# Performance work log

Measured on AMD Instinct MI355X. Metric: run time of the kernel, lower is better.

## Reference

```python
import jax, jax.numpy as jnp
import numpy as np
import math

H = 128          # node_dim == hidden_dim
TED = 128        # time_emb_dim
T = 64
BN = 4096


def _mlp(x, w1, b1, w2, b2):
    # 2-layer MLP with SiLU, matching MLP(n_layer=2, act_fn=SiLU)
    return jax.nn.silu(x @ w1 + b1) @ w2 + b2


def _timestep_embedding(t, dim):
    # get_timestep_embedding for possibly-negative relative indices
    half = dim // 2
    freqs = jnp.exp(jnp.arange(half, dtype=jnp.float32) * (-math.log(10000.0) / (half - 1)))
    arg = t.astype(jnp.float32)[:, None] * freqs[None, :]
    return jnp.concatenate([jnp.sin(arg), jnp.cos(arg)], axis=-1)


def setup_inputs() -> dict:
    key = jax.random.key(0)
    ks = jax.random.split(key, 20)
    s = 1.0 / math.sqrt(H)
    d = {
        "x": jax.random.normal(ks[0], (BN, 3, T), jnp.float32),
        "h": jax.random.normal(ks[1], (BN, H, T), jnp.float32),
        "q_w1": jax.random.normal(ks[2], (H, H), jnp.float32) * s,
        "q_b1": jnp.zeros((H,), jnp.float32),
        "q_w2": jax.random.normal(ks[3], (H, H), jnp.float32) * s,
        "q_b2": jnp.zeros((H,), jnp.float32),
        "k_w1": jax.random.normal(ks[4], (H, H), jnp.float32) * s,
        "k_b1": jnp.zeros((H,), jnp.float32),
        "k_w2": jax.random.normal(ks[5], (H, H), jnp.float32) * s,
        "k_b2": jnp.zeros((H,), jnp.float32),
        "v_w1": jax.random.normal(ks[6], (H, H), jnp.float32) * s,
        "v_b1": jnp.zeros((H,), jnp.float32),
        "v_w2": jax.random.normal(ks[7], (H, H), jnp.float32) * s,
        "v_b2": jnp.zeros((H,), jnp.float32),
        "xm_w1": jax.random.normal(ks[8], (H, H), jnp.float32) * s,
        "xm_b1": jnp.zeros((H,), jnp.float32),
        "xm_w2": jax.random.normal(ks[9], (H, 1), jnp.float32) * s,
        "xm_b2": jnp.zeros((1,), jnp.float32),
        "t_w": jax.random.normal(ks[10], (TED, H), jnp.float32) * (1.0 / math.sqrt(TED)),
        "t_b": jnp.zeros((H,), jnp.float32),
    }
    return d


def reference(x, h, q_w1, q_b1, q_w2, q_b2, k_w1, k_b1, k_w2, k_b2,
              v_w1, v_b1, v_w2, v_b2, xm_w1, xm_b1, xm_w2, xm_b2, t_w, t_b):
    Tn = x.shape[-1]
    # relative time embedding E[t, s, :] of shape [T, T, H]
    ti = jnp.arange(Tn)
    rel = (ti[:, None] - ti[None, :]).reshape(-1)
    E = (_timestep_embedding(rel, TED) @ t_w + t_b).reshape(Tn, Tn, -1)

    # merge_time_dim: [N, H, T] -> [N*T, H]  (token order: node-major, time-minor)
    tok = h.transpose(0, 2, 1)                      # [N, T, H]
    q = _mlp(tok, q_w1, q_b1, q_w2, q_b2)           # [N, T, H]
    k = _mlp(tok, k_w1, k_b1, k_w2, k_b2)           # [N, T, H]
    v = _mlp(tok, v_w1, v_b1, v_w2, v_b2)           # [N, T, H]
    vx = _mlp(v, xm_w1, xm_b1, xm_w2, xm_b2)[..., 0]  # [N, T]

    # scores: q . (k_s + E_ts)  -- decomposed, avoids materializing k_ts [N,H,T,T]
    scores = jnp.einsum('nth,nsh->nts', q, k) + jnp.einsum('nth,tsh->nts', q, E)
    alpha = jax.nn.softmax(scores, axis=-1)          # [N, T, S]

    # h update: sum_s alpha * (v_s + E_ts)
    dh = jnp.einsum('nts,nsh->nth', alpha, v) + jnp.einsum('nts,tsh->nth', alpha, E)
    h_out = h + dh.transpose(0, 2, 1)                # [N, H, T]

    # x update: x_t += sum_s alpha[t,s] * vx[s] * (x_t - x_s)
    w = alpha * vx[:, None, :]                       # [N, T, S]
    x_out = x + x * jnp.sum(w, axis=-1)[:, None, :] - jnp.einsum('nts,nds->ndt', w, x)
    return (x_out, h_out)
```

## Files before the change

kernel.cpp:

```cpp
#include <hip/hip_runtime.h>
#include <hip/hip_bf16.h>
#include <math.h>

#define NN 4096

typedef __attribute__((ext_vector_type(8))) short s8v;
typedef __attribute__((ext_vector_type(4))) float f4v;
typedef __attribute__((ext_vector_type(4))) unsigned int u32x4;
typedef __attribute__((ext_vector_type(2))) unsigned int u32x2;
typedef unsigned short u16;

static __device__ __forceinline__ f4v MFMA16(s8v a, s8v b, f4v c) {
  return __builtin_amdgcn_mfma_f32_16x16x32_bf16(a, b, c, 0, 0, 0);
}
static __device__ __forceinline__ u16 f2bf(float f) {
  union { float f; unsigned int u; } v; v.f = f;
  unsigned int r = v.u + 0x7fffu + ((v.u >> 16) & 1u);
  return (u16)(r >> 16);
}
static __device__ __forceinline__ float bf2f(u16 u) {
  union { unsigned int u; float f; } v; v.u = ((unsigned int)u) << 16;
  return v.f;
}
static __device__ __forceinline__ unsigned int cvt2u(float lo, float hi) {
  __hip_bfloat162 h = __float22bfloat162_rn(make_float2(lo, hi));
  union { __hip_bfloat162 b; unsigned int u; } c; c.b = h; return c.u;
}

#define SW(row, byte)  ((row) * 256 + ((byte) ^ (((row) & 7) << 4)))
#define SWH(row, byte) ((row) * 128 + ((byte) ^ (((row) & 7) << 4)))

__global__ void prep_kernel(const float* __restrict__ qw1, const float* __restrict__ qw2,
                            const float* __restrict__ kw1, const float* __restrict__ kw2,
                            const float* __restrict__ vw1, const float* __restrict__ vw2,
                            const float* __restrict__ xmw1,
                            const float* __restrict__ t_w, const float* __restrict__ t_b,
                            u16* __restrict__ wsb) {
  int b = blockIdx.x;
  if (b < 7) {
    const float* W;
    switch (b) {
      case 0: W = qw1; break; case 1: W = qw2; break;
      case 2: W = kw1; break; case 3: W = kw2; break;
      case 4: W = vw1; break; case 5: W = vw2; break;
      default: W = xmw1; break;
    }
    u16* o = wsb + b * 16384;
    for (int i = 0; i < 128; ++i) {
      int idx = i * 128 + threadIdx.x;
      int h = idx >> 7, c = idx & 127;
      o[c * 128 + h] = f2bf(W[idx]);
    }
  } else {
    int r = b - 7;
    int o = threadIdx.x;
    __shared__ float sc[128];
    float rel = (float)(r - 63);
    if (o < 64) {
      float f = expf((float)o * (-logf(10000.0f) / 63.0f));
      float a = rel * f;
      sc[o] = sinf(a);
      sc[o + 64] = cosf(a);
    }
    __syncthreads();
    float acc = t_b[o];
    for (int i = 0; i < 128; ++i) acc = fmaf(sc[i], t_w[i * 128 + o], acc);
    u16 bb = f2bf(acc);
    wsb[7 * 16384 + r * 128 + o] = bb;
    wsb[8 * 16384 + o * 128 + r] = bb;
  }
}

template <bool SILU, bool HASB, bool VT>
__device__ __forceinline__ void gemm128(const u16* __restrict__ Ag,
                                        const unsigned char* Bl,
                                        unsigned char* Ol,
                                        unsigned char* vTout,
                                        const float* __restrict__ bias,
                                        int w, int l) {
  const int lr = l & 15, lk = l >> 4;
  const int m0 = w * 16;
  float bj[4];
#pragma unroll
  for (int j = 0; j < 4; ++j) bj[j] = HASB ? bias[m0 + lk * 4 + j] : 0.f;
  f4v acc[4];
#pragma unroll
  for (int ni = 0; ni < 4; ++ni)
#pragma unroll
    for (int j = 0; j < 4; ++j) acc[ni][j] = bj[j];
#pragma unroll
  for (int kt = 0; kt < 4; ++kt) {
    s8v a = *(const s8v*)&Ag[(m0 + lr) * 128 + kt * 32 + lk * 8];
#pragma unroll
    for (int ni = 0; ni < 4; ++ni) {
      s8v b = *(const s8v*)(Bl + SW(ni * 16 + lr, kt * 64 + lk * 16));
      acc[ni] = MFMA16(a, b, acc[ni]);
    }
  }
#pragma unroll
  for (int ni = 0; ni < 4; ++ni) {
    int t = ni * 16 + lr;
    float v0 = acc[ni][0], v1 = acc[ni][1], v2 = acc[ni][2], v3 = acc[ni][3];
    if (SILU) {
      v0 *= __builtin_amdgcn_rcpf(1.0f + __expf(-v0));
      v1 *= __builtin_amdgcn_rcpf(1.0f + __expf(-v1));
      v2 *= __builtin_amdgcn_rcpf(1.0f + __expf(-v2));
      v3 *= __builtin_amdgcn_rcpf(1.0f + __expf(-v3));
    }
    unsigned int c0 = cvt2u(v0, v1), c1 = cvt2u(v2, v3);
    u32x2 st; st[0] = c0; st[1] = c1;
    *(u32x2*)(Ol + SW(t, m0 * 2 + lk * 8)) = st;
    if (VT) {
      *(u16*)(vTout + SWH(m0 + lk * 4 + 0, t * 2)) = (u16)(c0 & 0xffffu);
      *(u16*)(vTout + SWH(m0 + lk * 4 + 1, t * 2)) = (u16)(c0 >> 16);
      *(u16*)(vTout + SWH(m0 + lk * 4 + 2, t * 2)) = (u16)(c1 & 0xffffu);
      *(u16*)(vTout + SWH(m0 + lk * 4 + 3, t * 2)) = (u16)(c1 >> 16);
    }
  }
}

#define OFF_TOK 0
#define OFF_HID 16384
#define OFF_Q   32768
#define OFF_K   49152
#define OFF_VX  57344
#define OFF_XLS 57600
#define OFF_V   65536
#define SMEM_SZ 81920

__launch_bounds__(512, 4)
__global__ void et_main(const float* __restrict__ xg, const float* __restrict__ hg,
                        const u16* __restrict__ wsb,
                        const float* __restrict__ qb1, const float* __restrict__ qb2,
                        const float* __restrict__ kb1, const float* __restrict__ kb2,
                        const float* __restrict__ vb1, const float* __restrict__ vb2,
                        const float* __restrict__ xmb1, const float* __restrict__ xmw2,
                        const float* __restrict__ xmb2,
                        float* __restrict__ xout, float* __restrict__ hout) {
  __shared__ __align__(16) unsigned char smem[SMEM_SZ];
  unsigned char* TOK = smem + OFF_TOK;
  unsigned char* HID = smem + OFF_HID;
  unsigned char* QB  = smem + OFF_Q;
  unsigned char* KB  = smem + OFF_K;
  unsigned char* VB  = smem + OFF_V;
  unsigned char* VT  = TOK;
  unsigned char* SCO = HID;
  unsigned char* A2  = QB;
  unsigned char* ALP = KB;
  unsigned char* Y   = VB;
  float* vxb = (float*)(smem + OFF_VX);
  float* xls = (float*)(smem + OFF_XLS);

  const u16* WTq1 = wsb + 0 * 16384;
  const u16* WTq2 = wsb + 1 * 16384;
  const u16* WTk1 = wsb + 2 * 16384;
  const u16* WTk2 = wsb + 3 * 16384;
  const u16* WTv1 = wsb + 4 * 16384;
  const u16* WTv2 = wsb + 5 * 16384;
  const u16* WTxm = wsb + 6 * 16384;
  const u16* ErelB = wsb + 7 * 16384;
  const u16* ErelT = wsb + 8 * 16384;

  const int tid = threadIdx.x;
  const int l = tid & 63;
  const int w = __builtin_amdgcn_readfirstlane(tid >> 6);
  const int n = blockIdx.x;
  const size_t hbase = (size_t)n * 8192;

  {
    int t = tid & 63;
    int c0 = (tid >> 6) * 2;
#pragma unroll
    for (int cc = 0; cc < 2; ++cc) {
      int c = c0 + cc;
      float hv[8];
#pragma unroll
      for (int j = 0; j < 8; ++j) hv[j] = hg[hbase + (size_t)(c * 8 + j) * 64 + t];
      u32x4 pk;
#pragma unroll
      for (int j = 0; j < 4; ++j) pk[j] = cvt2u(hv[2 * j], hv[2 * j + 1]);
      *(u32x4*)(TOK + SW(t, c * 16)) = pk;
    }
  }
  __syncthreads();

  gemm128<true , true, false>(WTq1, TOK, HID, nullptr, qb1, w, l); __syncthreads();
  gemm128<false, true, false>(WTq2, HID, QB , nullptr, qb2, w, l); __syncthreads();
  gemm128<true , true, false>(WTk1, TOK, HID, nullptr, kb1, w, l); __syncthreads();
  gemm128<false, true, false>(WTk2, HID, KB , nullptr, kb2, w, l); __syncthreads();
  gemm128<true , true, false>(WTv1, TOK, HID, nullptr, vb1, w, l); __syncthreads();
  gemm128<false, true, true >(WTv2, HID, VB , VT     , vb2, w, l); __syncthreads();
  gemm128<true , true, false>(WTxm, VB , HID, nullptr, xmb1, w, l); __syncthreads();

  float vxreg;
  {
    int t = tid >> 3, g = tid & 7;
    s8v h0 = *(const s8v*)(HID + SW(t, g * 32));
    s8v h1 = *(const s8v*)(HID + SW(t, g * 32 + 16));
    float sum = 0.f;
#pragma unroll
    for (int c = 0; c < 8; ++c) sum = fmaf(bf2f((u16)h0[c]), xmw2[g * 16 + c], sum);
#pragma unroll
    for (int c = 0; c < 8; ++c) sum = fmaf(bf2f((u16)h1[c]), xmw2[g * 16 + 8 + c], sum);
    sum += __shfl_xor(sum, 1, 64);
    sum += __shfl_xor(sum, 2, 64);
    sum += __shfl_xor(sum, 4, 64);
    vxreg = sum;
  }
  gemm128<false, false, false>(ErelB, QB, VB, nullptr, nullptr, w, l);
  __syncthreads();

  {
    const int lr = l & 15, lk = l >> 4;
    const int m0 = (w & 3) * 16;
    const int n0 = (w >> 2) * 32;
    f4v acc[2];
#pragma unroll
    for (int ni = 0; ni < 2; ++ni)
#pragma unroll
      for (int j = 0; j < 4; ++j) acc[ni][j] = 0.f;
#pragma unroll
    for (int kt = 0; kt < 4; ++kt) {
      s8v a = *(const s8v*)(KB + SW(m0 + lr, kt * 64 + lk * 16));
#pragma unroll
      for (int ni = 0; ni < 2; ++ni) {
        s8v b = *(const s8v*)(QB + SW(n0 + ni * 16 + lr, kt * 64 + lk * 16));
        acc[ni] = MFMA16(a, b, acc[ni]);
      }
    }
#pragma unroll
    for (int ni = 0; ni < 2; ++ni) {
      int t = n0 + ni * 16 + lr;
      float4 out;
      float* op = (float*)&out;
#pragma unroll
      for (int j = 0; j < 4; ++j) {
        int s = m0 + lk * 4 + j;
        int r = t - s + 63;
        op[j] = acc[ni][j] + bf2f(*(const u16*)(VB + SW(t, r * 2)));
      }
      *(float4*)(SCO + SW(t, m0 * 4 + lk * 16)) = out;
    }
  }
  __syncthreads();

  unsigned int ac[4];
  {
    int t = tid >> 3, g = tid & 7;
    float4 v0 = *(float4*)(SCO + SW(t, g * 32));
    float4 v1 = *(float4*)(SCO + SW(t, g * 32 + 16));
    float e[8] = {v0.x, v0.y, v0.z, v0.w, v1.x, v1.y, v1.z, v1.w};
    float m = e[0];
#pragma unroll
    for (int i = 1; i < 8; ++i) m = fmaxf(m, e[i]);
    m = fmaxf(m, __shfl_xor(m, 1, 64));
    m = fmaxf(m, __shfl_xor(m, 2, 64));
    m = fmaxf(m, __shfl_xor(m, 4, 64));
    float s = 0.f;
#pragma unroll
    for (int i = 0; i < 8; ++i) { e[i] = __expf(e[i] - m); s += e[i]; }
    s += __shfl_xor(s, 1, 64);
    s += __shfl_xor(s, 2, 64);
    s += __shfl_xor(s, 4, 64);
    float inv = __builtin_amdgcn_rcpf(s);
#pragma unroll
    for (int i = 0; i < 4; ++i) ac[i] = cvt2u(e[2 * i] * inv, e[2 * i + 1] * inv);
    u32x4 st; st[0] = ac[0]; st[1] = ac[1]; st[2] = ac[2]; st[3] = ac[3];
    *(u32x4*)(ALP + SWH(t, g * 16)) = st;
    u32x4 zz; zz[0] = zz[1] = zz[2] = zz[3] = 0;
    *(u32x4*)(A2 + tid * 16) = zz;
    *(u32x4*)(A2 + 8192 + tid * 16) = zz;
    if (tid < 96) *(u32x4*)(Y + 512 + tid * 16) = zz;
    if ((tid & 7) == 0) vxb[t] = vxreg + xmb2[0];
    if (tid < 192) xls[tid] = xg[n * 192 + tid];
  }
  __syncthreads();

  {
    int t = tid >> 3, g = tid & 7;
    u16 ab[8];
#pragma unroll
    for (int i = 0; i < 4; ++i) { ab[2 * i] = (u16)(ac[i] & 0xffffu); ab[2 * i + 1] = (u16)(ac[i] >> 16); }
#pragma unroll
    for (int i = 0; i < 8; ++i) {
      int r = t + 63 - 8 * g - i;
      *(u16*)(A2 + SW(t, r * 2)) = ab[i];
    }
    if (tid >= 64 && tid < 128) {
      int s2 = tid - 64;
      float vv = vxb[s2];
      unsigned int p0 = cvt2u(vv, vv * xls[s2]);
      unsigned int p1 = cvt2u(vv * xls[64 + s2], vv * xls[128 + s2]);
      *(u16*)(Y + 0 * 128 + 2 * s2) = (u16)(p0 & 0xffffu);
      *(u16*)(Y + 1 * 128 + 2 * s2) = (u16)(p0 >> 16);
      *(u16*)(Y + 2 * 128 + 2 * s2) = (u16)(p1 & 0xffffu);
      *(u16*)(Y + 3 * 128 + 2 * s2) = (u16)(p1 >> 16);
    }
  }
  __syncthreads();

  {
    const int lr = l & 15, lk = l >> 4;
    const int m0 = w * 16;
    float hld[16];
#pragma unroll
    for (int ni = 0; ni < 4; ++ni) {
      size_t base = hbase + (size_t)(m0 + lk * 4) * 64 + ni * 16 + lr;
#pragma unroll
      for (int j = 0; j < 4; ++j) hld[ni * 4 + j] = hg[base + j * 64];
    }
    f4v acc[4];
#pragma unroll
    for (int ni = 0; ni < 4; ++ni)
#pragma unroll
      for (int j = 0; j < 4; ++j) acc[ni][j] = 0.f;
#pragma unroll
    for (int kt = 0; kt < 2; ++kt) {
      s8v a = *(const s8v*)(VT + SWH(m0 + lr, kt * 64 + lk * 16));
#pragma unroll
      for (int ni = 0; ni < 4; ++ni) {
        s8v b = *(const s8v*)(ALP + SWH(ni * 16 + lr, kt * 64 + lk * 16));
        acc[ni] = MFMA16(a, b, acc[ni]);
      }
    }
#pragma unroll
    for (int kt = 0; kt < 4; ++kt) {
      s8v a = *(const s8v*)&ErelT[(m0 + lr) * 128 + kt * 32 + lk * 8];
#pragma unroll
      for (int ni = 0; ni < 4; ++ni) {
        s8v b = *(const s8v*)(A2 + SW(ni * 16 + lr, kt * 64 + lk * 16));
        acc[ni] = MFMA16(a, b, acc[ni]);
      }
    }
#pragma unroll
    for (int ni = 0; ni < 4; ++ni) {
      size_t base = hbase + (size_t)(m0 + lk * 4) * 64 + ni * 16 + lr;
#pragma unroll
      for (int j = 0; j < 4; ++j) hout[base + j * 64] = hld[ni * 4 + j] + acc[ni][j];
    }

    if (w == 0) {
      f4v xa[4];
#pragma unroll
      for (int ni = 0; ni < 4; ++ni)
#pragma unroll
        for (int j = 0; j < 4; ++j) xa[ni][j] = 0.f;
#pragma unroll
      for (int kt = 0; kt < 2; ++kt) {
        s8v a = *(const s8v*)(Y + lr * 128 + kt * 64 + lk * 16);
#pragma unroll
        for (int ni = 0; ni < 4; ++ni) {
          s8v b = *(const s8v*)(ALP + SWH(ni * 16 + lr, kt * 64 + lk * 16));
          xa[ni] = MFMA16(a, b, xa[ni]);
        }
      }
      if (lk == 0) {
#pragma unroll
        for (int ni = 0; ni < 4; ++ni) {
          int t = ni * 16 + lr;
          float a1 = xa[ni][0];
#pragma unroll
          for (int d = 0; d < 3; ++d) {
            float xv = xls[d * 64 + t];
            xout[n * 192 + d * 64 + t] = fmaf(xv, a1, xv) - xa[ni][1 + d];
          }
        }
      }
    }
  }
}

extern "C" void kernel_launch(void* const* d_in, const int* in_sizes, int n_in,
                              void* d_out, int out_size, void* d_ws, size_t ws_size,
                              hipStream_t stream) {
  const float* xg   = (const float*)d_in[0];
  const float* hg   = (const float*)d_in[1];
  const float* qw1  = (const float*)d_in[2];
  const float* qb1  = (const float*)d_in[3];
  const float* qw2  = (const float*)d_in[4];
  const float* qb2  = (const float*)d_in[5];
  const float* kw1  = (const float*)d_in[6];
  const float* kb1  = (const float*)d_in[7];
  const float* kw2  = (const float*)d_in[8];
  const float* kb2  = (const float*)d_in[9];
  const float* vw1  = (const float*)d_in[10];
  const float* vb1  = (const float*)d_in[11];
  const float* vw2  = (const float*)d_in[12];
  const float* vb2  = (const float*)d_in[13];
  const float* xmw1 = (const float*)d_in[14];
  const float* xmb1 = (const float*)d_in[15];
  const float* xmw2 = (const float*)d_in[16];
  const float* xmb2 = (const float*)d_in[17];
  const float* t_w  = (const float*)d_in[18];
  const float* t_b  = (const float*)d_in[19];

  u16* wsb = (u16*)d_ws;
  float* xout = (float*)d_out;
  float* hout = xout + (size_t)NN * 192;

  prep_kernel<<<135, 128, 0, stream>>>(qw1, qw2, kw1, kw2, vw1, vw2, xmw1, t_w, t_b, wsb);
  et_main<<<NN, 512, 0, stream>>>(xg, hg, wsb,
                                  qb1, qb2, kb1, kb2, vb1, vb2, xmb1, xmw2, xmb2,
                                  xout, hout);
}
```

Measured before the change: 208.6 us.

## Batch MLP GEMMs per barrier with prepacked MFMA fragments and fused vx reduction

The weights and relative time embeddings are prepacked into MFMA fragment order, so each lane loads its A operand with one contiguous 16-byte read. The seven sequential GEMM stages, each followed by a barrier, are regrouped into three phases that each run independent GEMMs (q/k/v first layers together, then second layers), cutting the number of block barriers. The xm MLP output projection is fused into the GEMM epilogue with shuffle reductions instead of a separate pass, and the V transpose moves out of the GEMM epilogue into its own step. The x update is spread over four waves instead of one. The shared-memory layout is reorganised to fit these phases, which increases register pressure per wave.

```diff
diff --git a/kernel.cpp b/kernel.cpp
--- a/kernel.cpp
+++ b/kernel.cpp
@@ -30,73 +30,87 @@
 #define SW(row, byte)  ((row) * 256 + ((byte) ^ (((row) & 7) << 4)))
 #define SWH(row, byte) ((row) * 128 + ((byte) ^ (((row) & 7) << 4)))
 
-__global__ void prep_kernel(const float* __restrict__ qw1, const float* __restrict__ qw2,
-                            const float* __restrict__ kw1, const float* __restrict__ kw2,
-                            const float* __restrict__ vw1, const float* __restrict__ vw2,
+#define FA_OFF 0
+#define FB_OFF 49152
+#define FC_OFF 98304
+#define FD_OFF 131072
+
+__global__ void prep_kernel(const float* __restrict__ qw1, const float* __restrict__ kw1,
+                            const float* __restrict__ vw1, const float* __restrict__ qw2,
+                            const float* __restrict__ kw2, const float* __restrict__ vw2,
                             const float* __restrict__ xmw1,
                             const float* __restrict__ t_w, const float* __restrict__ t_b,
                             u16* __restrict__ wsb) {
-  int b = blockIdx.x;
-  if (b < 7) {
-    const float* W;
-    switch (b) {
-      case 0: W = qw1; break; case 1: W = qw2; break;
-      case 2: W = kw1; break; case 3: W = kw2; break;
-      case 4: W = vw1; break; case 5: W = vw2; break;
-      default: W = xmw1; break;
-    }
-    u16* o = wsb + b * 16384;
-    for (int i = 0; i < 128; ++i) {
-      int idx = i * 128 + threadIdx.x;
-      int h = idx >> 7, c = idx & 127;
-      o[c * 128 + h] = f2bf(W[idx]);
-    }
+  const int b = blockIdx.x, tid = threadIdx.x;
+  const int kt = tid >> 6, l = tid & 63, lr = l & 15, lk = l >> 4;
+  if (b < 56) {
+    const float* W; int mt; u16* base;
+    if (b < 24)      { base = wsb + FA_OFF; mt = b;      W = (b < 8) ? qw1 : (b < 16) ? kw1 : vw1; }
+    else if (b < 48) { base = wsb + FB_OFF; mt = b - 24; W = (mt < 8) ? qw2 : (mt < 16) ? kw2 : vw2; }
+    else             { base = wsb + FC_OFF; mt = b - 48; W = xmw1; }
+    const int ch = (mt & 7) * 16;
+    u16 o[8];
+#pragma unroll
+    for (int j = 0; j < 8; ++j) o[j] = f2bf(W[(kt * 32 + lk * 8 + j) * 128 + ch + lr]);
+    u32x4 pk;
+#pragma unroll
+    for (int i = 0; i < 4; ++i) pk[i] = (unsigned int)o[2 * i] | ((unsigned int)o[2 * i + 1] << 16);
+    *(u32x4*)&base[((mt * 4 + kt) * 64 + l) * 8] = pk;
   } else {
-    int r = b - 7;
-    int o = threadIdx.x;
-    __shared__ float sc[128];
-    float rel = (float)(r - 63);
-    if (o < 64) {
-      float f = expf((float)o * (-logf(10000.0f) / 63.0f));
+    const int rt = b - 56;
+    const int r = rt * 16 + lr;
+    const float rel = (float)(r - 63);
+    const int h0 = kt * 32 + lk * 8;
+    float acc[8];
+#pragma unroll
+    for (int j = 0; j < 8; ++j) acc[j] = t_b[h0 + j];
+    const float C = -logf(10000.0f) / 63.0f;
+    for (int i = 0; i < 64; ++i) {
+      float f = expf((float)i * C);
       float a = rel * f;
-      sc[o] = sinf(a);
-      sc[o + 64] = cosf(a);
-    }
-    __syncthreads();
-    float acc = t_b[o];
-    for (int i = 0; i < 128; ++i) acc = fmaf(sc[i], t_w[i * 128 + o], acc);
-    u16 bb = f2bf(acc);
-    wsb[7 * 16384 + r * 128 + o] = bb;
-    wsb[8 * 16384 + o * 128 + r] = bb;
-  }
-}
-
-template <bool SILU, bool HASB, bool VT>
-__device__ __forceinline__ void gemm128(const u16* __restrict__ Ag,
-                                        const unsigned char* Bl,
-                                        unsigned char* Ol,
-                                        unsigned char* vTout,
-                                        const float* __restrict__ bias,
-                                        int w, int l) {
+      float sn = sinf(a), cs = cosf(a);
+#pragma unroll
+      for (int j = 0; j < 8; ++j) acc[j] = fmaf(sn, t_w[i * 128 + h0 + j], acc[j]);
+#pragma unroll
+      for (int j = 0; j < 8; ++j) acc[j] = fmaf(cs, t_w[(i + 64) * 128 + h0 + j], acc[j]);
+    }
+    u16 o[8];
+#pragma unroll
+    for (int j = 0; j < 8; ++j) o[j] = f2bf(acc[j]);
+    u32x4 pk;
+#pragma unroll
+    for (int i = 0; i < 4; ++i) pk[i] = (unsigned int)o[2 * i] | ((unsigned int)o[2 * i + 1] << 16);
+    *(u32x4*)&wsb[FC_OFF + (((8 + rt) * 4 + kt) * 64 + l) * 8] = pk;
+    const int ct = h0 >> 4, lrp = h0 & 15;
+    const int ktp = r >> 5, lkp = (r >> 3) & 3, jp = r & 7;
+#pragma unroll
+    for (int j = 0; j < 8; ++j)
+      wsb[FD_OFF + ((ct * 4 + ktp) * 64 + lkp * 16 + lrp + j) * 8 + jp] = o[j];
+  }
+}
+
+template <bool SILU, bool HASB>
+__device__ __forceinline__ void tile_gemm(const u16* __restrict__ fr,
+                                          const unsigned char* Bl, unsigned char* Ol,
+                                          const float* __restrict__ bias,
+                                          int ocol, int l) {
   const int lr = l & 15, lk = l >> 4;
-  const int m0 = w * 16;
+  s8v a[4];
+#pragma unroll
+  for (int kt = 0; kt < 4; ++kt) a[kt] = *(const s8v*)&fr[(kt * 64 + l) * 8];
   float bj[4];
 #pragma unroll
-  for (int j = 0; j < 4; ++j) bj[j] = HASB ? bias[m0 + lk * 4 + j] : 0.f;
+  for (int j = 0; j < 4; ++j) bj[j] = HASB ? bias[lk * 4 + j] : 0.f;
   f4v acc[4];
 #pragma unroll
   for (int ni = 0; ni < 4; ++ni)
 #pragma unroll
     for (int j = 0; j < 4; ++j) acc[ni][j] = bj[j];
 #pragma unroll
-  for (int kt = 0; kt < 4; ++kt) {
-    s8v a = *(const s8v*)&Ag[(m0 + lr) * 128 + kt * 32 + lk * 8];
-#pragma unroll
-    for (int ni = 0; ni < 4; ++ni) {
-      s8v b = *(const s8v*)(Bl + SW(ni * 16 + lr, kt * 64 + lk * 16));
-      acc[ni] = MFMA16(a, b, acc[ni]);
-    }
-  }
+  for (int kt = 0; kt < 4; ++kt)
+#pragma unroll
+    for (int ni = 0; ni < 4; ++ni)
+      acc[ni] = MFMA16(a[kt], *(const s8v*)(Bl + SW(ni * 16 + lr, kt * 64 + lk * 16)), acc[ni]);
 #pragma unroll
   for (int ni = 0; ni < 4; ++ni) {
     int t = ni * 16 + lr;
@@ -107,26 +121,10 @@
       v2 *= __builtin_amdgcn_rcpf(1.0f + __expf(-v2));
       v3 *= __builtin_amdgcn_rcpf(1.0f + __expf(-v3));
     }
-    unsigned int c0 = cvt2u(v0, v1), c1 = cvt2u(v2, v3);
-    u32x2 st; st[0] = c0; st[1] = c1;
-    *(u32x2*)(Ol + SW(t, m0 * 2 + lk * 8)) = st;
-    if (VT) {
-      *(u16*)(vTout + SWH(m0 + lk * 4 + 0, t * 2)) = (u16)(c0 & 0xffffu);
-      *(u16*)(vTout + SWH(m0 + lk * 4 + 1, t * 2)) = (u16)(c0 >> 16);
-      *(u16*)(vTout + SWH(m0 + lk * 4 + 2, t * 2)) = (u16)(c1 & 0xffffu);
-      *(u16*)(vTout + SWH(m0 + lk * 4 + 3, t * 2)) = (u16)(c1 >> 16);
-    }
-  }
-}
-
-#define OFF_TOK 0
-#define OFF_HID 16384
-#define OFF_Q   32768
-#define OFF_K   49152
-#define OFF_VX  57344
-#define OFF_XLS 57600
-#define OFF_V   65536
-#define SMEM_SZ 81920
+    u32x2 st; st[0] = cvt2u(v0, v1); st[1] = cvt2u(v2, v3);
+    *(u32x2*)(Ol + SW(t, ocol + lk * 8)) = st;
+  }
+}
 
 __launch_bounds__(512, 4)
 __global__ void et_main(const float* __restrict__ xg, const float* __restrict__ hg,
@@ -137,39 +135,31 @@
                         const float* __restrict__ xmb1, const float* __restrict__ xmw2,
                         const float* __restrict__ xmb2,
                         float* __restrict__ xout, float* __restrict__ hout) {
-  __shared__ __align__(16) unsigned char smem[SMEM_SZ];
-  unsigned char* TOK = smem + OFF_TOK;
-  unsigned char* HID = smem + OFF_HID;
-  unsigned char* QB  = smem + OFF_Q;
-  unsigned char* KB  = smem + OFF_K;
-  unsigned char* VB  = smem + OFF_V;
-  unsigned char* VT  = TOK;
-  unsigned char* SCO = HID;
-  unsigned char* A2  = QB;
-  unsigned char* ALP = KB;
-  unsigned char* Y   = VB;
-  float* vxb = (float*)(smem + OFF_VX);
-  float* xls = (float*)(smem + OFF_XLS);
-
-  const u16* WTq1 = wsb + 0 * 16384;
-  const u16* WTq2 = wsb + 1 * 16384;
-  const u16* WTk1 = wsb + 2 * 16384;
-  const u16* WTk2 = wsb + 3 * 16384;
-  const u16* WTv1 = wsb + 4 * 16384;
-  const u16* WTv2 = wsb + 5 * 16384;
-  const u16* WTxm = wsb + 6 * 16384;
-  const u16* ErelB = wsb + 7 * 16384;
-  const u16* ErelT = wsb + 8 * 16384;
+  __shared__ __align__(16) unsigned char smem[81920];
+  unsigned char* S0 = smem;
+  unsigned char* S1 = smem + 16384;
+  unsigned char* S2 = smem + 32768;
+  unsigned char* S3 = smem + 49152;
+  unsigned char* S4 = smem + 65536;
+  unsigned char* ALP = S0;
+  unsigned char* YB  = S0 + 8192;
+  float* VXP = (float*)(S0 + 10240);
+  float* XLS = (float*)(S0 + 12288);
+
+  const u16* FA = wsb + FA_OFF;
+  const u16* FB = wsb + FB_OFF;
+  const u16* FC = wsb + FC_OFF;
+  const u16* FD = wsb + FD_OFF;
 
   const int tid = threadIdx.x;
   const int l = tid & 63;
+  const int lr = l & 15, lk = l >> 4;
   const int w = __builtin_amdgcn_readfirstlane(tid >> 6);
   const int n = blockIdx.x;
   const size_t hbase = (size_t)n * 8192;
 
   {
-    int t = tid & 63;
-    int c0 = (tid >> 6) * 2;
+    int t = tid & 63, c0 = (tid >> 6) * 2;
 #pragma unroll
     for (int cc = 0; cc < 2; ++cc) {
       int c = c0 + cc;
@@ -179,41 +169,59 @@
       u32x4 pk;
 #pragma unroll
       for (int j = 0; j < 4; ++j) pk[j] = cvt2u(hv[2 * j], hv[2 * j + 1]);
-      *(u32x4*)(TOK + SW(t, c * 16)) = pk;
-    }
-  }
-  __syncthreads();
-
-  gemm128<true , true, false>(WTq1, TOK, HID, nullptr, qb1, w, l); __syncthreads();
-  gemm128<false, true, false>(WTq2, HID, QB , nullptr, qb2, w, l); __syncthreads();
-  gemm128<true , true, false>(WTk1, TOK, HID, nullptr, kb1, w, l); __syncthreads();
-  gemm128<false, true, false>(WTk2, HID, KB , nullptr, kb2, w, l); __syncthreads();
-  gemm128<true , true, false>(WTv1, TOK, HID, nullptr, vb1, w, l); __syncthreads();
-  gemm128<false, true, true >(WTv2, HID, VB , VT     , vb2, w, l); __syncthreads();
-  gemm128<true , true, false>(WTxm, VB , HID, nullptr, xmb1, w, l); __syncthreads();
-
-  float vxreg;
-  {
-    int t = tid >> 3, g = tid & 7;
-    s8v h0 = *(const s8v*)(HID + SW(t, g * 32));
-    s8v h1 = *(const s8v*)(HID + SW(t, g * 32 + 16));
-    float sum = 0.f;
-#pragma unroll
-    for (int c = 0; c < 8; ++c) sum = fmaf(bf2f((u16)h0[c]), xmw2[g * 16 + c], sum);
-#pragma unroll
-    for (int c = 0; c < 8; ++c) sum = fmaf(bf2f((u16)h1[c]), xmw2[g * 16 + 8 + c], sum);
-    sum += __shfl_xor(sum, 1, 64);
-    sum += __shfl_xor(sum, 2, 64);
-    sum += __shfl_xor(sum, 4, 64);
-    vxreg = sum;
-  }
-  gemm128<false, false, false>(ErelB, QB, VB, nullptr, nullptr, w, l);
-  __syncthreads();
-
-  {
-    const int lr = l & 15, lk = l >> 4;
-    const int m0 = (w & 3) * 16;
-    const int n0 = (w >> 2) * 32;
+      *(u32x4*)(S0 + SW(t, c * 16)) = pk;
+    }
+  }
+  __syncthreads();
+
+  tile_gemm<true, true>(FA + (w)      * 2048, S0, S1, qb1 + w * 16, w * 32, l);
+  tile_gemm<true, true>(FA + (w + 8)  * 2048, S0, S2, kb1 + w * 16, w * 32, l);
+  tile_gemm<true, true>(FA + (w + 16) * 2048, S0, S3, vb1 + w * 16, w * 32, l);
+  __syncthreads();
+
+  tile_gemm<false, true>(FB + (w)     * 2048, S1, S4, qb2 + w * 16, w * 32, l);
+  tile_gemm<false, true>(FB + (w + 8) * 2048, S2, S0, kb2 + w * 16, w * 32, l);
+  __syncthreads();
+
+  tile_gemm<false, true >(FB + (w + 16) * 2048, S3, S1, vb2 + w * 16, w * 32, l);
+  tile_gemm<false, false>(FC + (w + 8)  * 2048, S4, S2, nullptr,      w * 32, l);
+  __syncthreads();
+
+  float vxr[4];
+  {
+    const u16* fx = FC + w * 2048;
+    s8v a[4];
+#pragma unroll
+    for (int kt = 0; kt < 4; ++kt) a[kt] = *(const s8v*)&fx[(kt * 64 + l) * 8];
+    float bj[4], w2[4];
+#pragma unroll
+    for (int j = 0; j < 4; ++j) { bj[j] = xmb1[w * 16 + lk * 4 + j]; w2[j] = xmw2[w * 16 + lk * 4 + j]; }
+    f4v acc[4];
+#pragma unroll
+    for (int ni = 0; ni < 4; ++ni)
+#pragma unroll
+      for (int j = 0; j < 4; ++j) acc[ni][j] = bj[j];
+#pragma unroll
+    for (int kt = 0; kt < 4; ++kt)
+#pragma unroll
+      for (int ni = 0; ni < 4; ++ni)
+        acc[ni] = MFMA16(a[kt], *(const s8v*)(S1 + SW(ni * 16 + lr, kt * 64 + lk * 16)), acc[ni]);
+#pragma unroll
+    for (int ni = 0; ni < 4; ++ni) {
+      float s = 0.f;
+#pragma unroll
+      for (int j = 0; j < 4; ++j) {
+        float v = acc[ni][j];
+        v *= __builtin_amdgcn_rcpf(1.0f + __expf(-v));
+        s = fmaf(v, w2[j], s);
+      }
+      s += __shfl_xor(s, 16, 64);
+      s += __shfl_xor(s, 32, 64);
+      vxr[ni] = s;
+    }
+  }
+  {
+    const int m0 = (w & 3) * 16, n0 = (w >> 2) * 32;
     f4v acc[2];
 #pragma unroll
     for (int ni = 0; ni < 2; ++ni)
@@ -221,12 +229,10 @@
       for (int j = 0; j < 4; ++j) acc[ni][j] = 0.f;
 #pragma unroll
     for (int kt = 0; kt < 4; ++kt) {
-      s8v a = *(const s8v*)(KB + SW(m0 + lr, kt * 64 + lk * 16));
-#pragma unroll
-      for (int ni = 0; ni < 2; ++ni) {
-        s8v b = *(const s8v*)(QB + SW(n0 + ni * 16 + lr, kt * 64 + lk * 16));
-        acc[ni] = MFMA16(a, b, acc[ni]);
-      }
+      s8v a = *(const s8v*)(S0 + SW(m0 + lr, kt * 64 + lk * 16));
+#pragma unroll
+      for (int ni = 0; ni < 2; ++ni)
+        acc[ni] = MFMA16(a, *(const s8v*)(S4 + SW(n0 + ni * 16 + lr, kt * 64 + lk * 16)), acc[ni]);
     }
 #pragma unroll
     for (int ni = 0; ni < 2; ++ni) {
@@ -236,10 +242,9 @@
 #pragma unroll
       for (int j = 0; j < 4; ++j) {
         int s = m0 + lk * 4 + j;
-        int r = t - s + 63;
-        op[j] = acc[ni][j] + bf2f(*(const u16*)(VB + SW(t, r * 2)));
+        op[j] = acc[ni][j] + bf2f(*(const u16*)(S2 + SW(t, (t - s + 63) * 2)));
       }
-      *(float4*)(SCO + SW(t, m0 * 4 + lk * 16)) = out;
+      *(float4*)(S3 + SW(t, m0 * 4 + lk * 16)) = out;
     }
   }
   __syncthreads();
@@ -247,8 +252,8 @@
   unsigned int ac[4];
   {
     int t = tid >> 3, g = tid & 7;
-    float4 v0 = *(float4*)(SCO + SW(t, g * 32));
-    float4 v1 = *(float4*)(SCO + SW(t, g * 32 + 16));
+    float4 v0 = *(float4*)(S3 + SW(t, g * 32));
+    float4 v1 = *(float4*)(S3 + SW(t, g * 32 + 16));
     float e[8] = {v0.x, v0.y, v0.z, v0.w, v1.x, v1.y, v1.z, v1.w};
     float m = e[0];
 #pragma unroll
@@ -268,11 +273,14 @@
     u32x4 st; st[0] = ac[0]; st[1] = ac[1]; st[2] = ac[2]; st[3] = ac[3];
     *(u32x4*)(ALP + SWH(t, g * 16)) = st;
     u32x4 zz; zz[0] = zz[1] = zz[2] = zz[3] = 0;
-    *(u32x4*)(A2 + tid * 16) = zz;
-    *(u32x4*)(A2 + 8192 + tid * 16) = zz;
-    if (tid < 96) *(u32x4*)(Y + 512 + tid * 16) = zz;
-    if ((tid & 7) == 0) vxb[t] = vxreg + xmb2[0];
-    if (tid < 192) xls[tid] = xg[n * 192 + tid];
+    *(u32x4*)(S4 + tid * 16) = zz;
+    *(u32x4*)(S4 + 8192 + tid * 16) = zz;
+    if (tid < 96) *(u32x4*)(YB + 512 + tid * 16) = zz;
+    if (l < 16) {
+#pragma unroll
+      for (int ni = 0; ni < 4; ++ni) VXP[w * 64 + ni * 16 + l] = vxr[ni];
+    }
+    if (tid < 192) XLS[tid] = xg[n * 192 + tid];
   }
   __syncthreads();
 
@@ -282,25 +290,39 @@
 #pragma unroll
     for (int i = 0; i < 4; ++i) { ab[2 * i] = (u16)(ac[i] & 0xffffu); ab[2 * i + 1] = (u16)(ac[i] >> 16); }
 #pragma unroll
-    for (int i = 0; i < 8; ++i) {
-      int r = t + 63 - 8 * g - i;
-      *(u16*)(A2 + SW(t, r * 2)) = ab[i];
-    }
-    if (tid >= 64 && tid < 128) {
-      int s2 = tid - 64;
-      float vv = vxb[s2];
-      unsigned int p0 = cvt2u(vv, vv * xls[s2]);
-      unsigned int p1 = cvt2u(vv * xls[64 + s2], vv * xls[128 + s2]);
-      *(u16*)(Y + 0 * 128 + 2 * s2) = (u16)(p0 & 0xffffu);
-      *(u16*)(Y + 1 * 128 + 2 * s2) = (u16)(p0 >> 16);
-      *(u16*)(Y + 2 * 128 + 2 * s2) = (u16)(p1 & 0xffffu);
-      *(u16*)(Y + 3 * 128 + 2 * s2) = (u16)(p1 >> 16);
-    }
-  }
-  __syncthreads();
-
-  {
-    const int lr = l & 15, lk = l >> 4;
+    for (int i = 0; i < 8; ++i)
+      *(u16*)(S4 + SW(t, (t + 63 - 8 * g - i) * 2)) = ab[i];
+  }
+  {
+    int c = ((w & 1) << 6) + l;
+    int t0 = (w >> 1) << 4;
+    u16 vt[16];
+#pragma unroll
+    for (int i = 0; i < 16; ++i) vt[i] = *(const u16*)(S1 + SW(t0 + i, c * 2));
+    u32x4 p0, p1;
+#pragma unroll
+    for (int i = 0; i < 4; ++i) {
+      p0[i] = (unsigned int)vt[2 * i]     | ((unsigned int)vt[2 * i + 1] << 16);
+      p1[i] = (unsigned int)vt[8 + 2 * i] | ((unsigned int)vt[9 + 2 * i] << 16);
+    }
+    *(u32x4*)(S2 + SWH(c, t0 * 2))      = p0;
+    *(u32x4*)(S2 + SWH(c, t0 * 2 + 16)) = p1;
+  }
+  if (tid < 64) {
+    float s = VXP[tid];
+#pragma unroll
+    for (int wv = 1; wv < 8; ++wv) s += VXP[wv * 64 + tid];
+    s += xmb2[0];
+    unsigned int p0 = cvt2u(s, s * XLS[tid]);
+    unsigned int p1 = cvt2u(s * XLS[64 + tid], s * XLS[128 + tid]);
+    *(u16*)(YB + SWH(0, 2 * tid)) = (u16)(p0 & 0xffffu);
+    *(u16*)(YB + SWH(1, 2 * tid)) = (u16)(p0 >> 16);
+    *(u16*)(YB + SWH(2, 2 * tid)) = (u16)(p1 & 0xffffu);
+    *(u16*)(YB + SWH(3, 2 * tid)) = (u16)(p1 >> 16);
+  }
+  __syncthreads();
+
+  {
     const int m0 = w * 16;
     float hld[16];
 #pragma unroll
@@ -316,21 +338,18 @@
       for (int j = 0; j < 4; ++j) acc[ni][j] = 0.f;
 #pragma unroll
     for (int kt = 0; kt < 2; ++kt) {
-      s8v a = *(const s8v*)(VT + SWH(m0 + lr, kt * 64 + lk * 16));
-#pragma unroll
-      for (int ni = 0; ni < 4; ++ni) {
-        s8v b = *(const s8v*)(ALP + SWH(ni * 16 + lr, kt * 64 + lk * 16));
-        acc[ni] = MFMA16(a, b, acc[ni]);
-      }
-    }
+      s8v a = *(const s8v*)(S2 + SWH(m0 + lr, kt * 64 + lk * 16));
+#pragma unroll
+      for (int ni = 0; ni < 4; ++ni)
+        acc[ni] = MFMA16(a, *(const s8v*)(ALP + SWH(ni * 16 + lr, kt * 64 + lk * 16)), acc[ni]);
+    }
+    const u16* fd = FD + w * 2048;
 #pragma unroll
     for (int kt = 0; kt < 4; ++kt) {
-      s8v a = *(const s8v*)&ErelT[(m0 + lr) * 128 + kt * 32 + lk * 8];
-#pragma unroll
-      for (int ni = 0; ni < 4; ++ni) {
-        s8v b = *(const s8v*)(A2 + SW(ni * 16 + lr, kt * 64 + lk * 16));
-        acc[ni] = MFMA16(a, b, acc[ni]);
-      }
+      s8v a = *(const s8v*)&fd[(kt * 64 + l) * 8];
+#pragma unroll
+      for (int ni = 0; ni < 4; ++ni)
+        acc[ni] = MFMA16(a, *(const s8v*)(S4 + SW(ni * 16 + lr, kt * 64 + lk * 16)), acc[ni]);
     }
 #pragma unroll
     for (int ni = 0; ni < 4; ++ni) {
@@ -338,32 +357,21 @@
 #pragma unroll
       for (int j = 0; j < 4; ++j) hout[base + j * 64] = hld[ni * 4 + j] + acc[ni][j];
     }
-
-    if (w == 0) {
-      f4v xa[4];
-#pragma unroll
-      for (int ni = 0; ni < 4; ++ni)
-#pragma unroll
-        for (int j = 0; j < 4; ++j) xa[ni][j] = 0.f;
-#pragma unroll
-      for (int kt = 0; kt < 2; ++kt) {
-        s8v a = *(const s8v*)(Y + lr * 128 + kt * 64 + lk * 16);
-#pragma unroll
-        for (int ni = 0; ni < 4; ++ni) {
-          s8v b = *(const s8v*)(ALP + SWH(ni * 16 + lr, kt * 64 + lk * 16));
-          xa[ni] = MFMA16(a, b, xa[ni]);
-        }
-      }
+    if (w < 4) {
+      f4v xa;
+#pragma unroll
+      for (int j = 0; j < 4; ++j) xa[j] = 0.f;
+#pragma unroll
+      for (int kt = 0; kt < 2; ++kt)
+        xa = MFMA16(*(const s8v*)(YB + SWH(lr, kt * 64 + lk * 16)),
+                    *(const s8v*)(ALP + SWH(w * 16 + lr, kt * 64 + lk * 16)), xa);
       if (lk == 0) {
-#pragma unroll
-        for (int ni = 0; ni < 4; ++ni) {
-          int t = ni * 16 + lr;
-          float a1 = xa[ni][0];
-#pragma unroll
-          for (int d = 0; d < 3; ++d) {
-            float xv = xls[d * 64 + t];
-            xout[n * 192 + d * 64 + t] = fmaf(xv, a1, xv) - xa[ni][1 + d];
-          }
+        int t = w * 16 + lr;
+        float a1 = xa[0];
+#pragma unroll
+        for (int d = 0; d < 3; ++d) {
+          float xv = XLS[d * 64 + t];
+          xout[n * 192 + d * 64 + t] = fmaf(xv, a1, xv) - xa[1 + d];
         }
       }
     }
@@ -398,7 +406,7 @@
   float* xout = (float*)d_out;
   float* hout = xout + (size_t)NN * 192;
 
-  prep_kernel<<<135, 128, 0, stream>>>(qw1, qw2, kw1, kw2, vw1, vw2, xmw1, t_w, t_b, wsb);
+  prep_kernel<<<64, 256, 0, stream>>>(qw1, kw1, vw1, qw2, kw2, vw2, xmw1, t_w, t_b, wsb);
   et_main<<<NN, 512, 0, stream>>>(xg, hg, wsb,
                                   qb1, qb2, kb1, kb2, vb1, vb2, xmb1, xmw2, xmb2,
                                   xout, hout);
```

Result: faster. 174.6 us (-16.3%).
